# Optimization experiments

Measured on AMD Instinct MI355X. Metric: run time of the kernel, lower is better.

## Reference

```python
import jax, jax.numpy as jnp
import numpy as np

B, C, H, W, HEADS = 8, 256, 128, 128, 8
HEADC = C // HEADS
EPS = 1e-5


def _ln(t, w, b):
    # per-head LayerNorm over the head-channel dim (last axis),
    # with per-head affine params of shape (heads, 1, headc)
    mu = jnp.mean(t, axis=-1, keepdims=True)
    var = jnp.mean(jnp.square(t - mu), axis=-1, keepdims=True)
    return (t - mu) * jax.lax.rsqrt(var + EPS) * w + b


def _forward(x, w_qkv, b_qkv, kln_w, kln_b, vln_w, vln_b, w_o1, b_o1, w_o2, b_o2):
    b, c, h, w = x.shape
    n = h * w
    heads, headc = kln_w.shape[0], c // kln_w.shape[0]
    # 1x1 conv qkv projection, channels-last output: [b,h,w,3c]
    qkv = jnp.einsum('bchw,oc->bhwo', x, w_qkv) + b_qkv
    qkv = qkv.reshape(b, n, heads, 3 * headc).transpose(0, 2, 1, 3)  # [b,heads,n,3*headc]
    q, k, v = jnp.split(qkv, 3, axis=-1)  # each [b,heads,n,headc]
    k = _ln(k, kln_w, kln_b)
    v = _ln(v, vln_w, vln_b)
    # Galerkin linear attention: (k^T v) then q @ (k^T v), normalized by n
    kv = jnp.einsum('bhnd,bhne->bhde', k, v) / n  # [b,heads,headc,headc]
    att = jnp.einsum('bhnd,bhde->bhne', q, kv)    # [b,heads,n,headc]
    att = att.transpose(0, 2, 1, 3).reshape(b, h, w, c).transpose(0, 3, 1, 2)
    ret = att + x
    y = jnp.einsum('bchw,oc->bohw', ret, w_o1) + b_o1[None, :, None, None]
    y = jax.nn.gelu(y, approximate=False)  # torch nn.GELU default = exact erf
    y = jnp.einsum('bchw,oc->bohw', y, w_o2) + b_o2[None, :, None, None]
    return y + x


def setup_inputs() -> dict:
    key = jax.random.key(0)
    ks = jax.random.split(key, 4)
    return {
        'x': jax.random.normal(ks[0], (B, C, H, W), dtype=jnp.float32),
        'w_qkv': jax.random.normal(ks[1], (3 * C, C), dtype=jnp.float32) * 0.02,
        'b_qkv': jnp.zeros((3 * C,), dtype=jnp.float32),
        'kln_w': jnp.ones((HEADS, 1, HEADC), dtype=jnp.float32),
        'kln_b': jnp.zeros((HEADS, 1, HEADC), dtype=jnp.float32),
        'vln_w': jnp.ones((HEADS, 1, HEADC), dtype=jnp.float32),
        'vln_b': jnp.zeros((HEADS, 1, HEADC), dtype=jnp.float32),
        'w_o1': jax.random.normal(ks[2], (C, C), dtype=jnp.float32) * 0.02,
        'b_o1': jnp.zeros((C,), dtype=jnp.float32),
        'w_o2': jax.random.normal(ks[3], (C, C), dtype=jnp.float32) * 0.02,
        'b_o2': jnp.zeros((C,), dtype=jnp.float32),
    }


def reference(x, w_qkv, b_qkv, kln_w, kln_b, vln_w, vln_b, w_o1, b_o1, w_o2, b_o2):
    return _forward(x, w_qkv, b_qkv, kln_w, kln_b, vln_w, vln_b, w_o1, b_o1, w_o2, b_o2)
```

## Files before the change

kernel.cpp:

```cpp
#include <hip/hip_runtime.h>
#include <hip/hip_bf16.h>
#include <cstdint>

typedef unsigned short u16;
typedef __attribute__((ext_vector_type(8))) short short8;
typedef __attribute__((ext_vector_type(4))) short short4v;
typedef __attribute__((ext_vector_type(4))) float f32x4;

#define HW_N 16384
#define CCH  256
#define BATCH 8
#define NHEAD 8
#define HEADC 32

static __device__ __forceinline__ float bf2f(u16 u){
    union { float f; uint32_t i; } x; x.i = ((uint32_t)u) << 16; return x.f;
}
static __device__ __forceinline__ u16 f2bf(float f){
    union { float f; uint32_t i; } x; x.f = f;
    uint32_t r = x.i + 0x7fffu + ((x.i >> 16) & 1u);
    return (u16)(r >> 16);
}

#define GLD16(gp, lp) __builtin_amdgcn_global_load_lds( \
    (const __attribute__((address_space(1))) uint32_t*)(gp), \
    (__attribute__((address_space(3))) uint32_t*)(lp), 16, 0, 0)

__global__ __launch_bounds__(256) void k_transpose_cast(const float* __restrict__ x,
                                                        u16* __restrict__ xb){
    __shared__ float tile[64][65];
    int b = blockIdx.z, ct = blockIdx.y, nt = blockIdx.x;
    int t = threadIdx.x;
    const float* src = x + ((size_t)b * CCH + ct * 64) * HW_N + nt * 64;
    #pragma unroll
    for (int it = 0; it < 16; ++it){
        int f = it * 256 + t;
        int i = f >> 6, j = f & 63;
        tile[i][j] = src[(size_t)i * HW_N + j];
    }
    __syncthreads();
    u16* dst = xb + ((size_t)b * HW_N + nt * 64) * CCH + ct * 64;
    #pragma unroll
    for (int it = 0; it < 16; ++it){
        int f = it * 256 + t;
        int jj = f >> 6, ii = f & 63;
        dst[(size_t)jj * CCH + ii] = f2bf(tile[ii][jj]);
    }
}

__global__ __launch_bounds__(256) void k_weight_prep(const float* __restrict__ w_qkv,
                                                     const float* __restrict__ b_qkv,
                                                     const float* __restrict__ w_o1,
                                                     const float* __restrict__ w_o2,
                                                     u16* __restrict__ wkv_b,
                                                     float* __restrict__ bkv_re,
                                                     u16* __restrict__ w_o1_b,
                                                     u16* __restrict__ w_o2_b){
    int id = blockIdx.x * 256 + threadIdx.x;
    if (id < 512 * 256){
        int r = id >> 8, c = id & 255;
        int h = r >> 6, s = (r >> 5) & 1, d = r & 31;
        int srow = h * 96 + 32 + s * 32 + d;
        wkv_b[id] = f2bf(w_qkv[(size_t)srow * 256 + c]);
        if (c == 0) bkv_re[r] = b_qkv[srow];
    } else {
        int id2 = id - 512 * 256;
        if (id2 < 65536)       w_o1_b[id2]         = f2bf(w_o1[id2]);
        else if (id2 < 131072) w_o2_b[id2 - 65536] = f2bf(w_o2[id2 - 65536]);
    }
}

__global__ __launch_bounds__(256, 2) void k_gemm_kv(const u16* __restrict__ A,
                                                    const u16* __restrict__ Bt,
                                                    const float* __restrict__ bkv,
                                                    const float* __restrict__ kln_w,
                                                    const float* __restrict__ kln_b,
                                                    const float* __restrict__ vln_w,
                                                    const float* __restrict__ vln_b,
                                                    float* __restrict__ kvpart){
    __shared__ __align__(16) u16 sh[16384];
    u16* lsA = sh;
    u16* lsB = sh + 8192;

    int lin = blockIdx.x + 4 * (blockIdx.y + 128 * blockIdx.z);
    int bx = (lin >> 3) & 3;
    int rest = (lin & 7) | ((lin >> 5) << 3);
    int by = rest & 127;
    int bz = rest >> 7;

    int row0 = bz * HW_N + by * 128;
    int col0 = bx * 128;

    int t = threadIdx.x;
    int wid = t >> 6, lane = t & 63;
    int wr = wid >> 1, wc = wid & 1;
    int q = lane >> 4, q4 = q * 4, lrow = lane & 15;

    f32x4 acc[4][4];
    #pragma unroll
    for (int i = 0; i < 4; ++i)
        #pragma unroll
        for (int j = 0; j < 4; ++j) acc[i][j] = (f32x4)0.0f;

    for (int kt = 0; kt < 4; ++kt){
        int c0 = kt * 64;
        #pragma unroll
        for (int it = 0; it < 4; ++it){
            int f  = it * 256 + t;
            int fs = f ^ ((f >> 3) & 7);
            int r  = f >> 3, c8 = (fs & 7) * 8;
            GLD16(&A [((size_t)(row0 + r)) * 256 + c0 + c8], &lsA[f * 8]);
            GLD16(&Bt[((size_t)(col0 + r)) * 256 + c0 + c8], &lsB[f * 8]);
        }
        __syncthreads();
        #pragma unroll
        for (int ks = 0; ks < 2; ++ks){
            int lk = q * 8 + ks * 32;
            short8 af[4], bfr[4];
            #pragma unroll
            for (int mi = 0; mi < 4; ++mi){
                int row = wr * 64 + mi * 16 + lrow;
                int e = (row * 64 + lk) ^ ((row & 7) << 3);
                af[mi] = *(const short8*)&lsA[e];
            }
            #pragma unroll
            for (int ni = 0; ni < 4; ++ni){
                int row = wc * 64 + ni * 16 + lrow;
                int e = (row * 64 + lk) ^ ((row & 7) << 3);
                bfr[ni] = *(const short8*)&lsB[e];
            }
            #pragma unroll
            for (int mi = 0; mi < 4; ++mi)
                #pragma unroll
                for (int ni = 0; ni < 4; ++ni)
                    acc[mi][ni] = __builtin_amdgcn_mfma_f32_16x16x32_bf16(
                        bfr[ni], af[mi], acc[mi][ni], 0, 0, 0);
        }
        __syncthreads();
    }

    int h = 2 * bx + wc;
    float bv[4][4], lwv[4][4], lbv[4][4];
    #pragma unroll
    for (int ni = 0; ni < 4; ++ni){
        const float* w  = (ni < 2) ? kln_w : vln_w;
        const float* bb = (ni < 2) ? kln_b : vln_b;
        #pragma unroll
        for (int r = 0; r < 4; ++r){
            int de = (ni & 1) * 16 + q4 + r;
            bv[ni][r]  = bkv[col0 + wc * 64 + ni * 16 + q4 + r];
            lwv[ni][r] = w[h * 32 + de];
            lbv[ni][r] = bb[h * 32 + de];
        }
    }

    #pragma unroll
    for (int mi = 0; mi < 4; ++mi){
        float ks = 0.f, ksq = 0.f, vs = 0.f, vsq = 0.f;
        #pragma unroll
        for (int ni = 0; ni < 4; ++ni)
            #pragma unroll
            for (int r = 0; r < 4; ++r){
                float t2 = acc[mi][ni][r] + bv[ni][r];
                acc[mi][ni][r] = t2;
                if (ni < 2){ ks += t2; ksq += t2 * t2; }
                else       { vs += t2; vsq += t2 * t2; }
            }
        ks  += __shfl_xor(ks, 16);  ks  += __shfl_xor(ks, 32);
        ksq += __shfl_xor(ksq, 16); ksq += __shfl_xor(ksq, 32);
        vs  += __shfl_xor(vs, 16);  vs  += __shfl_xor(vs, 32);
        vsq += __shfl_xor(vsq, 16); vsq += __shfl_xor(vsq, 32);
        float muk = ks * 0.03125f, muv = vs * 0.03125f;
        float rsk = rsqrtf(fmaxf(ksq * 0.03125f - muk * muk, 0.f) + 1e-5f);
        float rsv = rsqrtf(fmaxf(vsq * 0.03125f - muv * muv, 0.f) + 1e-5f);
        int n = wr * 64 + mi * 16 + lrow;
        #pragma unroll
        for (int ni = 0; ni < 4; ++ni){
            float mu = (ni < 2) ? muk : muv;
            float rs = (ni < 2) ? rsk : rsv;
            #pragma unroll
            for (int r = 0; r < 4; ++r){
                int d = (ni & 1) * 16 + q4 + r;
                float val = (acc[mi][ni][r] - mu) * rs * lwv[ni][r] + lbv[ni][r];
                int byteoff = ((wc * 2 + (ni >> 1)) << 13) + (d << 8) + (n << 1);
                byteoff ^= (d & 7) << 4;
                *(u16*)((char*)sh + byteoff) = f2bf(val);
            }
        }
    }
    __syncthreads();

    if (wid < 2){
        f32x4 a2[2][2];
        #pragma unroll
        for (int i = 0; i < 2; ++i)
            #pragma unroll
            for (int j = 0; j < 2; ++j) a2[i][j] = (f32x4)0.0f;
        #pragma unroll
        for (int ks2 = 0; ks2 < 4; ++ks2){
            int n0 = q * 8 + ks2 * 32;
            short8 kf[2], vf[2];
            #pragma unroll
            for (int mi = 0; mi < 2; ++mi){
                int d = mi * 16 + lrow;
                int bko = ((wid * 2 + 0) << 13) + (d << 8) + (n0 << 1);
                int bvo = ((wid * 2 + 1) << 13) + (d << 8) + (n0 << 1);
                bko ^= (d & 7) << 4;
                bvo ^= (d & 7) << 4;
                kf[mi] = *(const short8*)((char*)sh + bko);
                vf[mi] = *(const short8*)((char*)sh + bvo);
            }
            #pragma unroll
            for (int mi = 0; mi < 2; ++mi)
                #pragma unroll
                for (int ni = 0; ni < 2; ++ni)
                    a2[mi][ni] = __builtin_amdgcn_mfma_f32_16x16x32_bf16(
                        kf[mi], vf[ni], a2[mi][ni], 0, 0, 0);
        }
        float* dst = kvpart + (((size_t)(bz * 128 + by)) * 8 + 2 * bx + wid) * 1024;
        #pragma unroll
        for (int mi = 0; mi < 2; ++mi)
            #pragma unroll
            for (int ni = 0; ni < 2; ++ni)
                #pragma unroll
                for (int r = 0; r < 4; ++r)
                    dst[(mi * 16 + q4 + r) * 32 + ni * 16 + lrow] = a2[mi][ni][r];
    }
}

__global__ __launch_bounds__(256) void k_wqeff(const float* __restrict__ kvpart,
                                               const float* __restrict__ w_qkv,
                                               const float* __restrict__ b_qkv,
                                               u16* __restrict__ wq_eff_b,
                                               float* __restrict__ beff){
    __shared__ float kv[1024];
    int h = blockIdx.x, b = blockIdx.y;
    int t = threadIdx.x;
    f32x4 s = (f32x4)0.0f;
    for (int p = 0; p < 128; ++p){
        f32x4 v = *(const f32x4*)(kvpart + (((size_t)b * 128 + p) * 8 + h) * 1024 + t * 4);
        s = s + v;
    }
    const float invN = 1.0f / (float)HW_N;
    #pragma unroll
    for (int i = 0; i < 4; ++i) kv[t * 4 + i] = s[i] * invN;
    __syncthreads();

    float wcol[32];
    #pragma unroll
    for (int d = 0; d < 32; ++d)
        wcol[d] = w_qkv[((size_t)(h * 96 + d)) * 256 + t];
    for (int e = 0; e < 32; ++e){
        float s2 = 0.f;
        #pragma unroll
        for (int d = 0; d < 32; ++d) s2 += wcol[d] * kv[d * 32 + e];
        wq_eff_b[(((size_t)b * 256) + h * 32 + e) * 256 + t] = f2bf(s2);
    }
    if (t < 32){
        float s3 = 0.f;
        #pragma unroll
        for (int d = 0; d < 32; ++d) s3 += b_qkv[h * 96 + d] * kv[d * 32 + t];
        beff[b * 256 + h * 32 + t] = s3;
    }
}

#define STAGE_B(BT, KT, BUF) do {                                             \
    _Pragma("unroll")                                                         \
    for (int it_ = 0; it_ < 2; ++it_){                                        \
        int f_ = it_ * 512 + t;                                               \
        int o_ = f_ >> 2, sl_ = f_ & 3;                                       \
        GLD16(&(BT)[(size_t)o_ * 256 + (KT) * 32 + (sl_ ^ ((o_ >> 1) & 3)) * 8],\
              &(BUF)[f_ * 8]);                                                \
    }                                                                         \
} while(0)

#define ZACC do {                                                             \
    _Pragma("unroll") for (int i_ = 0; i_ < 4; ++i_)                          \
    _Pragma("unroll") for (int j_ = 0; j_ < 2; ++j_)                          \
        acc[i_][j_] = (f32x4)0.0f;                                            \
} while(0)

#define GEMM_STAGE_PIPE(BT, SWAPPED) do {                                     \
    _Pragma("unroll")                                                         \
    for (int kt = 0; kt < 8; ++kt){                                           \
        int cur = kt & 1;                                                     \
        if (kt < 7){                                                          \
            STAGE_B(BT, kt + 1, Bs[cur ^ 1]);                                 \
            asm volatile("s_waitcnt vmcnt(2)" ::: "memory");                  \
        } else {                                                              \
            asm volatile("s_waitcnt vmcnt(0)" ::: "memory");                  \
        }                                                                     \
        __builtin_amdgcn_s_barrier();                                         \
        __builtin_amdgcn_sched_barrier(0);                                    \
        short8 af[4], bf[2];                                                  \
        _Pragma("unroll")                                                     \
        for (int ni = 0; ni < 2; ++ni){                                       \
            int o_ = wid * 32 + ni * 16 + lrow;                               \
            bf[ni] = *(const short8*)((const char*)Bs[cur] + o_ * 64          \
                                      + ((q ^ ((o_ >> 1) & 3)) << 4));        \
        }                                                                     \
        _Pragma("unroll")                                                     \
        for (int mi = 0; mi < 4; ++mi){                                       \
            int n_ = mi * 16 + lrow;                                          \
            int sl_ = (kt * 4 + q) ^ (n_ & 7);                                \
            af[mi] = *(const short8*)((const char*)I + n_ * 512 + (sl_ << 4));\
        }                                                                     \
        __builtin_amdgcn_s_setprio(1);                                        \
        _Pragma("unroll")                                                     \
        for (int mi = 0; mi < 4; ++mi)                                        \
            _Pragma("unroll")                                                 \
            for (int ni = 0; ni < 2; ++ni)                                    \
                acc[mi][ni] = (SWAPPED)                                       \
                    ? __builtin_amdgcn_mfma_f32_16x16x32_bf16(                \
                          bf[ni], af[mi], acc[mi][ni], 0, 0, 0)               \
                    : __builtin_amdgcn_mfma_f32_16x16x32_bf16(                \
                          af[mi], bf[ni], acc[mi][ni], 0, 0, 0);              \
        __builtin_amdgcn_s_setprio(0);                                        \
        __builtin_amdgcn_s_barrier();                                         \
    }                                                                         \
} while(0)

#define LDS_FENCE_BARRIER() do {                                              \
    asm volatile("s_waitcnt lgkmcnt(0)" ::: "memory");                        \
    __builtin_amdgcn_s_barrier();                                             \
    __builtin_amdgcn_sched_barrier(0);                                        \
} while(0)

__global__ __launch_bounds__(512, 4) void k_fused3(const u16* __restrict__ xb,
                                                   const u16* __restrict__ wq_effb,
                                                   const float* __restrict__ beff,
                                                   const u16* __restrict__ w_o1_b,
                                                   const float* __restrict__ b_o1,
                                                   const u16* __restrict__ w_o2_b,
                                                   const float* __restrict__ b_o2,
                                                   const float* __restrict__ x,
                                                   float* __restrict__ out){
    __shared__ __align__(16) u16 I[16384];
    __shared__ __align__(16) u16 Bs[2][8192];

    int d = blockIdx.x;
    int bz = d & 7, nb = d >> 3;
    size_t row0 = (size_t)bz * HW_N + (size_t)nb * 64;

    int t = threadIdx.x, wid = t >> 6, lane = t & 63;
    int lrow = lane & 15, q = lane >> 4, q4 = q * 4;

    const u16* B1 = wq_effb + (size_t)bz * 65536;

    #pragma unroll
    for (int it = 0; it < 4; ++it){
        int f = it * 512 + t;
        int n = f >> 5, slot = f & 31;
        GLD16(&xb[(row0 + n) * 256 + (size_t)((slot ^ (n & 7)) * 8)], &I[f * 8]);
    }
    STAGE_B(B1, 0, Bs[0]);

    f32x4 acc[4][2];

    ZACC;
    GEMM_STAGE_PIPE(B1, true);
    STAGE_B(w_o1_b, 0, Bs[0]);
    #pragma unroll
    for (int ni = 0; ni < 2; ++ni){
        int o0 = wid * 32 + ni * 16 + q4;
        f32x4 be = *(const f32x4*)&beff[bz * 256 + o0];
        #pragma unroll
        for (int mi = 0; mi < 4; ++mi){
            int n = mi * 16 + lrow;
            int byte = (n * 512 + o0 * 2) ^ ((n & 7) << 4);
            short4v rv = *(const short4v*)((const char*)I + byte);
            short4v pk;
            #pragma unroll
            for (int r = 0; r < 4; ++r)
                pk[r] = (short)f2bf(acc[mi][ni][r] + be[r] + bf2f((u16)rv[r]));
            *(short4v*)((char*)I + byte) = pk;
        }
    }
    LDS_FENCE_BARRIER();

    ZACC;
    GEMM_STAGE_PIPE(w_o1_b, true);
    STAGE_B(w_o2_b, 0, Bs[0]);
    #pragma unroll
    for (int ni = 0; ni < 2; ++ni){
        int o0 = wid * 32 + ni * 16 + q4;
        f32x4 bo = *(const f32x4*)&b_o1[o0];
        #pragma unroll
        for (int mi = 0; mi < 4; ++mi){
            int n = mi * 16 + lrow;
            int byte = (n * 512 + o0 * 2) ^ ((n & 7) << 4);
            short4v pk;
            #pragma unroll
            for (int r = 0; r < 4; ++r){
                float v = acc[mi][ni][r] + bo[r];
                v = 0.5f * v * (1.0f + erff(v * 0.70710678118654752f));
                pk[r] = (short)f2bf(v);
            }
            *(short4v*)((char*)I + byte) = pk;
        }
    }
    LDS_FENCE_BARRIER();

    ZACC;
    GEMM_STAGE_PIPE(w_o2_b, false);
    #pragma unroll
    for (int ni = 0; ni < 2; ++ni){
        int o = wid * 32 + ni * 16 + lrow;
        float bo = b_o2[o];
        size_t base = ((size_t)bz * 256 + o) * HW_N + (size_t)nb * 64;
        #pragma unroll
        for (int mi = 0; mi < 4; ++mi){
            int n0 = mi * 16 + q4;
            f32x4 xv = *(const f32x4*)&x[base + n0];
            f32x4 ov;
            #pragma unroll
            for (int r = 0; r < 4; ++r) ov[r] = acc[mi][ni][r] + bo + xv[r];
            *(f32x4*)&out[base + n0] = ov;
        }
    }
}

extern "C" void kernel_launch(void* const* d_in, const int* in_sizes, int n_in,
                              void* d_out, int out_size, void* d_ws, size_t ws_size,
                              hipStream_t stream){
    const float* x     = (const float*)d_in[0];
    const float* w_qkv = (const float*)d_in[1];
    const float* b_qkv = (const float*)d_in[2];
    const float* kln_w = (const float*)d_in[3];
    const float* kln_b = (const float*)d_in[4];
    const float* vln_w = (const float*)d_in[5];
    const float* vln_b = (const float*)d_in[6];
    const float* w_o1  = (const float*)d_in[7];
    const float* b_o1  = (const float*)d_in[8];
    const float* w_o2  = (const float*)d_in[9];
    const float* b_o2  = (const float*)d_in[10];
    float* out = (float*)d_out;

    const size_t MB = 1u << 20;
    if (ws_size < 266 * MB) return;

    char* ws = (char*)d_ws;
    u16*   xb      = (u16*)(ws);
    float* kvpart  = (float*)(ws + 192 * MB);
    char*  sm      = ws + 264 * MB;
    u16*   wkv_b   = (u16*)sm;
    float* bkv_re  = (float*)(sm + 256 * 1024);
    u16*   w_o1_b  = (u16*)(sm + 260 * 1024);
    u16*   w_o2_b  = (u16*)(sm + 392 * 1024);
    u16*   wq_effb = (u16*)(sm + 524 * 1024);
    float* beff    = (float*)(sm + 1572 * 1024);

    k_transpose_cast<<<dim3(HW_N / 64, CCH / 64, BATCH), 256, 0, stream>>>(x, xb);
    k_weight_prep<<<dim3(1024), 256, 0, stream>>>(w_qkv, b_qkv, w_o1, w_o2,
                                                  wkv_b, bkv_re, w_o1_b, w_o2_b);
    k_gemm_kv<<<dim3(4, 128, BATCH), 256, 0, stream>>>(
        xb, wkv_b, bkv_re, kln_w, kln_b, vln_w, vln_b, kvpart);
    k_wqeff<<<dim3(NHEAD, BATCH), 256, 0, stream>>>(kvpart, w_qkv, b_qkv, wq_effb, beff);
    k_fused3<<<dim3(2048), 512, 0, stream>>>(
        xb, wq_effb, beff, w_o1_b, b_o1, w_o2_b, b_o2, x, out);
}
```

Measured before the change: 242.6 us.

## Double-buffer LDS tiles in KV GEMM to overlap global loads with MFMA

```diff
diff --git a/kernel.cpp b/kernel.cpp
--- a/kernel.cpp
+++ b/kernel.cpp
@@ -78,9 +78,7 @@
                                                     const float* __restrict__ vln_w,
                                                     const float* __restrict__ vln_b,
                                                     float* __restrict__ kvpart){
-    __shared__ __align__(16) u16 sh[16384];
-    u16* lsA = sh;
-    u16* lsB = sh + 8192;
+    __shared__ __align__(16) u16 sh[32768];
 
     int lin = blockIdx.x + 4 * (blockIdx.y + 128 * blockIdx.z);
     int bx = (lin >> 3) & 3;
@@ -102,17 +100,33 @@
         #pragma unroll
         for (int j = 0; j < 4; ++j) acc[i][j] = (f32x4)0.0f;
 
+#define STAGE_KV(C0, BASE) do {                                               \
+    _Pragma("unroll")                                                         \
+    for (int it_ = 0; it_ < 4; ++it_){                                        \
+        int f_  = it_ * 256 + t;                                              \
+        int fs_ = f_ ^ ((f_ >> 3) & 7);                                       \
+        int r_  = f_ >> 3, c8_ = (fs_ & 7) * 8;                               \
+        GLD16(&A [((size_t)(row0 + r_)) * 256 + (C0) + c8_],                  \
+              &sh[(BASE) + f_ * 8]);                                          \
+        GLD16(&Bt[((size_t)(col0 + r_)) * 256 + (C0) + c8_],                  \
+              &sh[(BASE) + 8192 + f_ * 8]);                                   \
+    }                                                                         \
+} while(0)
+
+    STAGE_KV(0, 0);
+    #pragma unroll
     for (int kt = 0; kt < 4; ++kt){
-        int c0 = kt * 64;
-        #pragma unroll
-        for (int it = 0; it < 4; ++it){
-            int f  = it * 256 + t;
-            int fs = f ^ ((f >> 3) & 7);
-            int r  = f >> 3, c8 = (fs & 7) * 8;
-            GLD16(&A [((size_t)(row0 + r)) * 256 + c0 + c8], &lsA[f * 8]);
-            GLD16(&Bt[((size_t)(col0 + r)) * 256 + c0 + c8], &lsB[f * 8]);
-        }
-        __syncthreads();
+        int cur = kt & 1;
+        if (kt < 3){
+            STAGE_KV((kt + 1) * 64, (cur ^ 1) * 16384);
+            asm volatile("s_waitcnt vmcnt(8)" ::: "memory");
+        } else {
+            asm volatile("s_waitcnt vmcnt(0)" ::: "memory");
+        }
+        __builtin_amdgcn_s_barrier();
+        __builtin_amdgcn_sched_barrier(0);
+        const u16* lsA = sh + cur * 16384;
+        const u16* lsB = sh + cur * 16384 + 8192;
         #pragma unroll
         for (int ks = 0; ks < 2; ++ks){
             int lk = q * 8 + ks * 32;
@@ -129,14 +143,16 @@
                 int e = (row * 64 + lk) ^ ((row & 7) << 3);
                 bfr[ni] = *(const short8*)&lsB[e];
             }
+            __builtin_amdgcn_s_setprio(1);
             #pragma unroll
             for (int mi = 0; mi < 4; ++mi)
                 #pragma unroll
                 for (int ni = 0; ni < 4; ++ni)
                     acc[mi][ni] = __builtin_amdgcn_mfma_f32_16x16x32_bf16(
                         bfr[ni], af[mi], acc[mi][ni], 0, 0, 0);
-        }
-        __syncthreads();
+            __builtin_amdgcn_s_setprio(0);
+        }
+        __builtin_amdgcn_s_barrier();
     }
 
     int h = 2 * bx + wc;
```

Measured after the change: 248.8 us. 2.5% more time.
